# Performance work log

Measured on AMD Instinct MI355X. Metric: run time of the kernel, lower is better.

Reference implementation:

```python
import jax, jax.numpy as jnp
import numpy as np

B, N, E, H = 2, 2048, 768, 12
D = E // H          # head_dim = 64
G = 16              # gate_dim
LN_EPS = 1e-5


def setup_inputs() -> dict:
    key = jax.random.key(0)
    ks = jax.random.split(key, 8)
    s = E ** -0.5
    x = jax.random.normal(ks[0], (B, N, E), jnp.float32)
    # per-head negative decay slopes (ALiBi/TNL-style)
    log_slope = -(2.0 ** (-8.0 * (jnp.arange(H, dtype=jnp.float32) + 1.0) / H))
    Wq = jax.random.normal(ks[1], (E, E), jnp.float32) * s
    Wk = jax.random.normal(ks[2], (E, E), jnp.float32) * s
    Wv = jax.random.normal(ks[3], (E, E), jnp.float32) * s
    Wo = jax.random.normal(ks[4], (E, E), jnp.float32) * s
    Wg1 = jax.random.normal(ks[5], (E, G), jnp.float32) * s
    Wg2 = jax.random.normal(ks[6], (G, E), jnp.float32) * (G ** -0.5)
    ln_w = jnp.ones((E,), jnp.float32)
    ln_b = jnp.zeros((E,), jnp.float32)
    return {"x": x, "log_slope": log_slope, "Wq": Wq, "Wk": Wk, "Wv": Wv,
            "Wo": Wo, "Wg1": Wg1, "Wg2": Wg2, "ln_w": ln_w, "ln_b": ln_b}


def _layernorm(x, w, b):
    mu = jnp.mean(x, axis=-1, keepdims=True)
    var = jnp.mean(jnp.square(x - mu), axis=-1, keepdims=True)
    return (x - mu) * jax.lax.rsqrt(var + LN_EPS) * w + b


def reference(x, log_slope, Wq, Wk, Wv, Wo, Wg1, Wg2, ln_w, ln_b):
    b, n, e = x.shape
    h = log_slope.shape[0]
    d = e // h
    silu = jax.nn.silu
    q = silu(x @ Wq).reshape(b, n, h, d).transpose(0, 2, 1, 3)  # b h n d
    k = silu(x @ Wk).reshape(b, n, h, d).transpose(0, 2, 1, 3)
    v = silu(x @ Wv).reshape(b, n, h, d).transpose(0, 2, 1, 3)

    # exp-decay causal mask: exp(log_slope * (i - j)) for i >= j, else 0
    idx = jnp.arange(n, dtype=jnp.float32)
    diff = idx[:, None] - idx[None, :]                    # n x m
    keep = diff >= 0
    decay = jnp.where(keep,
                      jnp.exp(log_slope[:, None, None] * jnp.maximum(diff, 0.0)),
                      0.0)                                # h n m

    energy = jnp.einsum('bhnd,bhmd->bhnm', q, k) * decay  # b h n m
    out = jnp.einsum('bhnm,bhmd->bhnd', energy, v)        # b h n d
    out = out.transpose(0, 2, 1, 3).reshape(b, n, e)

    gate = jax.nn.sigmoid((x @ Wg1) @ Wg2)                # low-rank output gate
    out = out * gate
    out = out @ Wo
    out = _layernorm(out, ln_w, ln_b)                     # norm_pos='post'
    return out
```

## Files before the change

kernel.cpp:

```cpp
#include <hip/hip_runtime.h>
#include <stdint.h>

#define BB 2
#define NN 2048
#define EE 768
#define HH 12
#define DD 64
#define GG 16

typedef unsigned short u16;
typedef unsigned int u32;
typedef __attribute__((ext_vector_type(8))) short short8;
typedef __attribute__((ext_vector_type(4))) float f32x4;
typedef __attribute__((ext_vector_type(4))) unsigned short u16x4;

__device__ __forceinline__ u16 f2bf(float f) {
  union { float f; u32 u; } a; a.f = f;
  u32 r = a.u + 0x7FFFu + ((a.u >> 16) & 1u);
  return (u16)(r >> 16);
}

__device__ __forceinline__ float silu_f(float v) { return v / (1.f + __expf(-v)); }

__device__ __forceinline__ void gload16(const u16* g, char* l) {
  __builtin_amdgcn_global_load_lds(
      (const __attribute__((address_space(1))) void*)(g),
      (__attribute__((address_space(3))) void*)(l), 16, 0, 0);
}

template<int ROWS>
__device__ __forceinline__ void stage_tile(const u16* __restrict__ gb, int ld, int row0, int col0,
                                           char* lds, int tid) {
  int wid = tid >> 6;
#pragma unroll
  for (int it = 0; it < ROWS / 32; ++it) {
    int c = it * 256 + tid;
    int r = c >> 3;
    int g = (c & 7) ^ (r & 7);
    gload16(gb + (size_t)(row0 + r) * ld + col0 + g * 8,
            lds + (it * 256 + wid * 64) * 16);
  }
}

__device__ __forceinline__ short8 read_frag(const char* lds, int row, int gk) {
  return *(const short8*)(lds + (((row << 3) | (gk ^ (row & 7))) << 4));
}

__global__ __launch_bounds__(256) void xconv_kernel(const float* __restrict__ x, u16* __restrict__ xb) {
  int i = blockIdx.x * 256 + threadIdx.x;
  float4 v = ((const float4*)x)[i];
  u16x4 o;
  o.x = f2bf(v.x); o.y = f2bf(v.y); o.z = f2bf(v.z); o.w = f2bf(v.w);
  ((u16x4*)xb)[i] = o;
}

__global__ __launch_bounds__(256) void wconv_kernel(const float* __restrict__ Wq, const float* __restrict__ Wk,
    const float* __restrict__ Wv, const float* __restrict__ Wo,
    u16* __restrict__ Wqt, u16* __restrict__ Wkt, u16* __restrict__ Wvt, u16* __restrict__ Wot) {
  const float* src; u16* dst;
  int z = blockIdx.z;
  if (z == 0)      { src = Wq; dst = Wqt; }
  else if (z == 1) { src = Wk; dst = Wkt; }
  else if (z == 2) { src = Wv; dst = Wvt; }
  else             { src = Wo; dst = Wot; }
  __shared__ float tb[64][65];
  int k0 = blockIdx.x * 64, n0 = blockIdx.y * 64;
  int tid = threadIdx.x;
#pragma unroll
  for (int i = 0; i < 16; ++i) {
    int idx = i * 256 + tid;
    int r = idx >> 6, c = idx & 63;
    tb[r][c] = src[(size_t)(k0 + r) * EE + n0 + c];
  }
  __syncthreads();
#pragma unroll
  for (int i = 0; i < 16; ++i) {
    int idx = i * 256 + tid;
    int rn = idx >> 6, ck = idx & 63;
    dst[(size_t)(n0 + rn) * EE + k0 + ck] = f2bf(tb[ck][rn]);
  }
}

__global__ __launch_bounds__(256) void tg_kernel(const float* __restrict__ x, const float* __restrict__ Wg1,
                                                 float* __restrict__ tg) {
  int tid = threadIdx.x, lane = tid & 63, wid = tid >> 6;
  int m = blockIdx.x * 4 + wid;
  int col = lane & 15, sl = lane >> 4;
  const float* xr = x + (size_t)m * EE + sl * 192;
  float acc = 0.f;
#pragma unroll 4
  for (int i = 0; i < 48; ++i) {
    float4 xv = ((const float4*)xr)[i];
    int kk = sl * 192 + i * 4;
    acc += xv.x * Wg1[(kk + 0) * GG + col];
    acc += xv.y * Wg1[(kk + 1) * GG + col];
    acc += xv.z * Wg1[(kk + 2) * GG + col];
    acc += xv.w * Wg1[(kk + 3) * GG + col];
  }
  acc += __shfl_down(acc, 32);
  acc += __shfl_down(acc, 16);
  if (lane < 16) tg[(size_t)m * GG + col] = acc;
}

__global__ __launch_bounds__(256) void qkv_gemm(const u16* __restrict__ xb,
    const u16* __restrict__ Wqt, const u16* __restrict__ Wkt, const u16* __restrict__ Wvt,
    u16* __restrict__ qp, u16* __restrict__ kp, u16* __restrict__ vtp) {
  __shared__ __attribute__((aligned(16))) char As[16384];
  __shared__ __attribute__((aligned(16))) char Zs[16384];
  int tid = threadIdx.x, lane = tid & 63, wid = tid >> 6;
  int m0 = blockIdx.x * 128, n0 = blockIdx.y * 128, w = blockIdx.z;
  const u16* Zt = (w == 0) ? Wqt : (w == 1) ? Wkt : Wvt;
  int wm = wid >> 1, wn = wid & 1;
  f32x4 acc[4][4] = {};
  for (int kt = 0; kt < EE / 64; ++kt) {
    __syncthreads();
    stage_tile<128>(xb, EE, m0, kt * 64, As, tid);
    stage_tile<128>(Zt, EE, n0, kt * 64, Zs, tid);
    __syncthreads();
    short8 af[2][4], bfr[2][4];
#pragma unroll
    for (int ds = 0; ds < 2; ++ds) {
      int gk = ds * 4 + (lane >> 4);
#pragma unroll
      for (int i = 0; i < 4; ++i) {
        af[ds][i]  = read_frag(As, wm * 64 + i * 16 + (lane & 15), gk);
        bfr[ds][i] = read_frag(Zs, wn * 64 + i * 16 + (lane & 15), gk);
      }
    }
#pragma unroll
    for (int mi = 0; mi < 4; ++mi)
#pragma unroll
      for (int ni = 0; ni < 4; ++ni) {
        acc[mi][ni] = __builtin_amdgcn_mfma_f32_16x16x32_bf16(af[0][mi], bfr[0][ni], acc[mi][ni], 0, 0, 0);
        acc[mi][ni] = __builtin_amdgcn_mfma_f32_16x16x32_bf16(af[1][mi], bfr[1][ni], acc[mi][ni], 0, 0, 0);
      }
  }
#pragma unroll
  for (int mi = 0; mi < 4; ++mi) {
    int mbase = m0 + wm * 64 + mi * 16 + ((lane >> 4) << 2);
    int bidx = mbase >> 11, nbase = mbase & 2047;
#pragma unroll
    for (int ni = 0; ni < 4; ++ni) {
      int e = n0 + wn * 64 + ni * 16 + (lane & 15);
      int h = e >> 6, d = e & 63;
      if (w < 2) {
        u16* dst = (w == 0 ? qp : kp) + (size_t)(bidx * HH + h) * NN * DD + d;
#pragma unroll
        for (int r = 0; r < 4; ++r)
          dst[(size_t)(nbase + r) * DD] = f2bf(silu_f(acc[mi][ni][r]));
      } else {
        u16x4 pk;
        pk.x = f2bf(silu_f(acc[mi][ni][0]));
        pk.y = f2bf(silu_f(acc[mi][ni][1]));
        pk.z = f2bf(silu_f(acc[mi][ni][2]));
        pk.w = f2bf(silu_f(acc[mi][ni][3]));
        *(u16x4*)(vtp + (size_t)((bidx * HH + h) * DD + d) * NN + nbase) = pk;
      }
    }
  }
}

__global__ __launch_bounds__(256) void attn_kernel(const u16* __restrict__ qp, const u16* __restrict__ kp,
    const u16* __restrict__ vtp, const float* __restrict__ slopes, float* __restrict__ attn) {
  __shared__ __attribute__((aligned(16))) char Ks[8192];
  __shared__ __attribute__((aligned(16))) char Vs[8192];
  __shared__ __attribute__((aligned(16))) char Ps[4][2304];
  int tid = threadIdx.x, lane = tid & 63, wid = tid >> 6;
  int q0 = blockIdx.x * 64;
  int bh = blockIdx.y, b = bh / HH, h = bh % HH;
  float slope = slopes[h];
  const u16* qbh = qp + (size_t)bh * NN * DD;
  const u16* kbh = kp + (size_t)bh * NN * DD;
  const u16* vbh = vtp + (size_t)bh * DD * NN;

  int qrow = q0 + wid * 16 + (lane & 15);
  short8 qf0 = *(const short8*)(qbh + (size_t)qrow * DD + ((lane >> 4) << 3));
  short8 qf1 = *(const short8*)(qbh + (size_t)qrow * DD + 32 + ((lane >> 4) << 3));

  f32x4 oacc[4] = {};
  float window = 30.f / (-slope);
  float jminf = (float)q0 - window;
  int kt_min = (jminf <= 0.f) ? 0 : (((int)jminf) >> 6);
  int kt_max = q0 >> 6;
  char* Pw = Ps[wid];

  for (int kt = kt_min; kt <= kt_max; ++kt) {
    __syncthreads();
    stage_tile<64>(kbh, DD, kt * 64, 0, Ks, tid);
    stage_tile<64>(vbh, NN, 0, kt * 64, Vs, tid);
    __syncthreads();
#pragma unroll
    for (int jt = 0; jt < 4; ++jt) {
      f32x4 s = {};
      s = __builtin_amdgcn_mfma_f32_16x16x32_bf16(qf0, read_frag(Ks, jt * 16 + (lane & 15), (lane >> 4)), s, 0, 0, 0);
      s = __builtin_amdgcn_mfma_f32_16x16x32_bf16(qf1, read_frag(Ks, jt * 16 + (lane & 15), 4 + (lane >> 4)), s, 0, 0, 0);
      int jg = kt * 64 + jt * 16 + (lane & 15);
#pragma unroll
      for (int r = 0; r < 4; ++r) {
        int qi = q0 + wid * 16 + ((lane >> 4) << 2) + r;
        int diff = qi - jg;
        float val = (diff >= 0) ? s[r] * __expf(slope * (float)diff) : 0.f;
        *(u16*)(Pw + ((((lane >> 4) << 2) + r) * 72 + jt * 16 + (lane & 15)) * 2) = f2bf(val);
      }
    }
    __syncthreads();
#pragma unroll
    for (int ks = 0; ks < 2; ++ks) {
      short8 pf = *(const short8*)(Pw + (lane & 15) * 144 + ks * 64 + ((lane >> 4) << 4));
#pragma unroll
      for (int dt = 0; dt < 4; ++dt) {
        oacc[dt] = __builtin_amdgcn_mfma_f32_16x16x32_bf16(
            pf, read_frag(Vs, dt * 16 + (lane & 15), ks * 4 + (lane >> 4)), oacc[dt], 0, 0, 0);
      }
    }
  }
#pragma unroll
  for (int dt = 0; dt < 4; ++dt) {
#pragma unroll
    for (int r = 0; r < 4; ++r) {
      int qi = q0 + wid * 16 + ((lane >> 4) << 2) + r;
      int e = h * 64 + dt * 16 + (lane & 15);
      attn[(size_t)(b * NN + qi) * EE + e] = oacc[dt][r];
    }
  }
}

__global__ __launch_bounds__(256) void gate_kernel(const float* __restrict__ attn, const float* __restrict__ tg,
    const float* __restrict__ Wg2, u16* __restrict__ gated) {
  int m0 = blockIdx.x * 8;
  __shared__ float ts[8][16];
  int tid = threadIdx.x;
  if (tid < 128) ts[tid >> 4][tid & 15] = tg[(size_t)(m0 + (tid >> 4)) * GG + (tid & 15)];
  __syncthreads();
  for (int e = tid; e < EE; e += 256) {
    float wv[16];
#pragma unroll
    for (int g = 0; g < 16; ++g) wv[g] = Wg2[g * EE + e];
#pragma unroll
    for (int r = 0; r < 8; ++r) {
      float gg = 0.f;
#pragma unroll
      for (int g = 0; g < 16; ++g) gg += ts[r][g] * wv[g];
      float sg = 1.f / (1.f + __expf(-gg));
      gated[(size_t)(m0 + r) * EE + e] = f2bf(attn[(size_t)(m0 + r) * EE + e] * sg);
    }
  }
}

__global__ __launch_bounds__(256) void wo_gemm(const u16* __restrict__ A, const u16* __restrict__ Zt,
                                               float* __restrict__ Y) {
  __shared__ __attribute__((aligned(16))) char As[16384];
  __shared__ __attribute__((aligned(16))) char Zs[16384];
  int tid = threadIdx.x, lane = tid & 63, wid = tid >> 6;
  int m0 = blockIdx.x * 128, n0 = blockIdx.y * 128;
  int wm = wid >> 1, wn = wid & 1;
  f32x4 acc[4][4] = {};
  for (int kt = 0; kt < EE / 64; ++kt) {
    __syncthreads();
    stage_tile<128>(A, EE, m0, kt * 64, As, tid);
    stage_tile<128>(Zt, EE, n0, kt * 64, Zs, tid);
    __syncthreads();
    short8 af[2][4], bfr[2][4];
#pragma unroll
    for (int ds = 0; ds < 2; ++ds) {
      int gk = ds * 4 + (lane >> 4);
#pragma unroll
      for (int i = 0; i < 4; ++i) {
        af[ds][i]  = read_frag(As, wm * 64 + i * 16 + (lane & 15), gk);
        bfr[ds][i] = read_frag(Zs, wn * 64 + i * 16 + (lane & 15), gk);
      }
    }
#pragma unroll
    for (int mi = 0; mi < 4; ++mi)
#pragma unroll
      for (int ni = 0; ni < 4; ++ni) {
        acc[mi][ni] = __builtin_amdgcn_mfma_f32_16x16x32_bf16(af[0][mi], bfr[0][ni], acc[mi][ni], 0, 0, 0);
        acc[mi][ni] = __builtin_amdgcn_mfma_f32_16x16x32_bf16(af[1][mi], bfr[1][ni], acc[mi][ni], 0, 0, 0);
      }
  }
#pragma unroll
  for (int mi = 0; mi < 4; ++mi) {
    int mbase = m0 + wm * 64 + mi * 16 + ((lane >> 4) << 2);
#pragma unroll
    for (int ni = 0; ni < 4; ++ni) {
      int e = n0 + wn * 64 + ni * 16 + (lane & 15);
#pragma unroll
      for (int r = 0; r < 4; ++r)
        Y[(size_t)(mbase + r) * EE + e] = acc[mi][ni][r];
    }
  }
}

__global__ __launch_bounds__(256) void ln_kernel(const float* __restrict__ y, const float* __restrict__ w,
    const float* __restrict__ bb, float* __restrict__ out) {
  int m = blockIdx.x, tid = threadIdx.x;
  const float* yr = y + (size_t)m * EE;
  float v0 = yr[tid], v1 = yr[tid + 256], v2 = yr[tid + 512];
  float s = v0 + v1 + v2;
  float s2 = v0 * v0 + v1 * v1 + v2 * v2;
#pragma unroll
  for (int off = 32; off > 0; off >>= 1) {
    s += __shfl_down(s, off);
    s2 += __shfl_down(s2, off);
  }
  __shared__ float ss[4], ssq[4];
  int lane = tid & 63, wid = tid >> 6;
  if (lane == 0) { ss[wid] = s; ssq[wid] = s2; }
  __syncthreads();
  s = ss[0] + ss[1] + ss[2] + ss[3];
  s2 = ssq[0] + ssq[1] + ssq[2] + ssq[3];
  float mu = s * (1.f / 768.f);
  float var = s2 * (1.f / 768.f) - mu * mu;
  float rs = rsqrtf(var + 1e-5f);
  float* orow = out + (size_t)m * EE;
  orow[tid]       = (v0 - mu) * rs * w[tid]       + bb[tid];
  orow[tid + 256] = (v1 - mu) * rs * w[tid + 256] + bb[tid + 256];
  orow[tid + 512] = (v2 - mu) * rs * w[tid + 512] + bb[tid + 512];
}

extern "C" void kernel_launch(void* const* d_in, const int* in_sizes, int n_in,
                              void* d_out, int out_size, void* d_ws, size_t ws_size,
                              hipStream_t stream) {
  (void)in_sizes; (void)n_in; (void)out_size; (void)ws_size;
  const float* x   = (const float*)d_in[0];
  const float* ls  = (const float*)d_in[1];
  const float* Wq  = (const float*)d_in[2];
  const float* Wk  = (const float*)d_in[3];
  const float* Wv  = (const float*)d_in[4];
  const float* Wo  = (const float*)d_in[5];
  const float* Wg1 = (const float*)d_in[6];
  const float* Wg2 = (const float*)d_in[7];
  const float* lnw = (const float*)d_in[8];
  const float* lnb = (const float*)d_in[9];

  char* p = (char*)d_ws;
  u16* xb   = (u16*)(p + 0);
  u16* Wqt  = (u16*)(p + 6291456);
  u16* Wkt  = (u16*)(p + 7471104);
  u16* Wvt  = (u16*)(p + 8650752);
  u16* Wot  = (u16*)(p + 9830400);
  u16* qq   = (u16*)(p + 11010048);
  u16* kk   = (u16*)(p + 17301504);
  u16* vt   = (u16*)(p + 23592960);
  float* tg = (float*)(p + 29884416);
  float* at = (float*)(p + 30146560);
  u16* gated = xb;
  float* yy = (float*)(p + 11010048);
  float* out = (float*)d_out;

  hipLaunchKernelGGL(xconv_kernel, dim3(3072), dim3(256), 0, stream, x, xb);
  hipLaunchKernelGGL(wconv_kernel, dim3(12, 12, 4), dim3(256), 0, stream, Wq, Wk, Wv, Wo, Wqt, Wkt, Wvt, Wot);
  hipLaunchKernelGGL(tg_kernel, dim3(1024), dim3(256), 0, stream, x, Wg1, tg);
  hipLaunchKernelGGL(qkv_gemm, dim3(32, 6, 3), dim3(256), 0, stream, xb, Wqt, Wkt, Wvt, qq, kk, vt);
  hipLaunchKernelGGL(attn_kernel, dim3(32, 24), dim3(256), 0, stream, qq, kk, vt, ls, at);
  hipLaunchKernelGGL(gate_kernel, dim3(512), dim3(256), 0, stream, at, tg, Wg2, gated);
  hipLaunchKernelGGL(wo_gemm, dim3(32, 6), dim3(256), 0, stream, gated, Wot, yy);
  hipLaunchKernelGGL(ln_kernel, dim3(4096), dim3(256), 0, stream, yy, lnw, lnb, out);
}
```

Before: 203.4 us.

## Split attention key range across blocks with atomic accumulation and factored decay

Adds a split-K dimension to the attention grid, where each block handles up to 8 key tiles for one query tile and combines partial outputs with atomicAdd into a pre-zeroed buffer. A new zero kernel clears that buffer first. The per-element exp is factored into a per-row term times a per-column term, and the intra-wave barrier before the P·V step becomes an LDS waitcnt. This targets load imbalance and low parallelism in the causal windowed loop, at the cost of an extra zeroing pass, atomic contention, and float-order nondeterminism; the factored exp may also overflow or underflow for large windows.

```diff
diff --git a/kernel.cpp b/kernel.cpp
--- a/kernel.cpp
+++ b/kernel.cpp
@@ -52,6 +52,10 @@
   u16x4 o;
   o.x = f2bf(v.x); o.y = f2bf(v.y); o.z = f2bf(v.z); o.w = f2bf(v.w);
   ((u16x4*)xb)[i] = o;
+}
+
+__global__ __launch_bounds__(256) void zero_kernel(float4* __restrict__ p) {
+  p[blockIdx.x * 256 + threadIdx.x] = float4{0.f, 0.f, 0.f, 0.f};
 }
 
 __global__ __launch_bounds__(256) void wconv_kernel(const float* __restrict__ Wq, const float* __restrict__ Wk,
@@ -160,50 +164,61 @@
   }
 }
 
+#define CH 8
 __global__ __launch_bounds__(256) void attn_kernel(const u16* __restrict__ qp, const u16* __restrict__ kp,
     const u16* __restrict__ vtp, const float* __restrict__ slopes, float* __restrict__ attn) {
   __shared__ __attribute__((aligned(16))) char Ks[8192];
   __shared__ __attribute__((aligned(16))) char Vs[8192];
   __shared__ __attribute__((aligned(16))) char Ps[4][2304];
   int tid = threadIdx.x, lane = tid & 63, wid = tid >> 6;
-  int q0 = blockIdx.x * 64;
-  int bh = blockIdx.y, b = bh / HH, h = bh % HH;
+  int q0 = blockIdx.y * 64;
+  int bh = blockIdx.z, b = bh / HH, h = bh % HH;
   float slope = slopes[h];
-  const u16* qbh = qp + (size_t)bh * NN * DD;
-  const u16* kbh = kp + (size_t)bh * NN * DD;
-  const u16* vbh = vtp + (size_t)bh * DD * NN;
-
-  int qrow = q0 + wid * 16 + (lane & 15);
-  short8 qf0 = *(const short8*)(qbh + (size_t)qrow * DD + ((lane >> 4) << 3));
-  short8 qf1 = *(const short8*)(qbh + (size_t)qrow * DD + 32 + ((lane >> 4) << 3));
-
-  f32x4 oacc[4] = {};
   float window = 30.f / (-slope);
   float jminf = (float)q0 - window;
   int kt_min = (jminf <= 0.f) ? 0 : (((int)jminf) >> 6);
   int kt_max = q0 >> 6;
+  int k0 = kt_min + (int)blockIdx.x * CH;
+  if (k0 > kt_max) return;
+  int k1 = min(k0 + CH - 1, kt_max);
+  bool single = (kt_max - kt_min) < CH;
+
+  const u16* qbh = qp + (size_t)bh * NN * DD;
+  const u16* kbh = kp + (size_t)bh * NN * DD;
+  const u16* vbh = vtp + (size_t)bh * DD * NN;
+
+  int qbase = q0 + wid * 16 + ((lane >> 4) << 2);
+  int qrow = q0 + wid * 16 + (lane & 15);
+  short8 qf0 = *(const short8*)(qbh + (size_t)qrow * DD + ((lane >> 4) << 3));
+  short8 qf1 = *(const short8*)(qbh + (size_t)qrow * DD + 32 + ((lane >> 4) << 3));
+
+  f32x4 oacc[4] = {};
   char* Pw = Ps[wid];
 
-  for (int kt = kt_min; kt <= kt_max; ++kt) {
+  for (int kt = k0; kt <= k1; ++kt) {
     __syncthreads();
     stage_tile<64>(kbh, DD, kt * 64, 0, Ks, tid);
     stage_tile<64>(vbh, NN, 0, kt * 64, Vs, tid);
     __syncthreads();
+    float t_hi = (float)(kt * 64 + 63);
+    float rex[4];
+#pragma unroll
+    for (int r = 0; r < 4; ++r) rex[r] = __expf(slope * ((float)(qbase + r) - t_hi));
 #pragma unroll
     for (int jt = 0; jt < 4; ++jt) {
       f32x4 s = {};
       s = __builtin_amdgcn_mfma_f32_16x16x32_bf16(qf0, read_frag(Ks, jt * 16 + (lane & 15), (lane >> 4)), s, 0, 0, 0);
       s = __builtin_amdgcn_mfma_f32_16x16x32_bf16(qf1, read_frag(Ks, jt * 16 + (lane & 15), 4 + (lane >> 4)), s, 0, 0, 0);
       int jg = kt * 64 + jt * 16 + (lane & 15);
+      float cex = __expf(slope * (t_hi - (float)jg));
 #pragma unroll
       for (int r = 0; r < 4; ++r) {
-        int qi = q0 + wid * 16 + ((lane >> 4) << 2) + r;
-        int diff = qi - jg;
-        float val = (diff >= 0) ? s[r] * __expf(slope * (float)diff) : 0.f;
+        int diff = qbase + r - jg;
+        float val = (diff >= 0) ? s[r] * rex[r] * cex : 0.f;
         *(u16*)(Pw + ((((lane >> 4) << 2) + r) * 72 + jt * 16 + (lane & 15)) * 2) = f2bf(val);
       }
     }
-    __syncthreads();
+    __asm__ volatile("s_waitcnt lgkmcnt(0)" ::: "memory");
 #pragma unroll
     for (int ks = 0; ks < 2; ++ks) {
       short8 pf = *(const short8*)(Pw + (lane & 15) * 144 + ks * 64 + ((lane >> 4) << 4));
@@ -218,9 +233,11 @@
   for (int dt = 0; dt < 4; ++dt) {
 #pragma unroll
     for (int r = 0; r < 4; ++r) {
-      int qi = q0 + wid * 16 + ((lane >> 4) << 2) + r;
+      int qi = qbase + r;
       int e = h * 64 + dt * 16 + (lane & 15);
-      attn[(size_t)(b * NN + qi) * EE + e] = oacc[dt][r];
+      float* dst = attn + (size_t)(b * NN + qi) * EE + e;
+      if (single) *dst = oacc[dt][r];
+      else atomicAdd(dst, oacc[dt][r]);
     }
   }
 }
@@ -349,10 +366,11 @@
   float* out = (float*)d_out;
 
   hipLaunchKernelGGL(xconv_kernel, dim3(3072), dim3(256), 0, stream, x, xb);
+  hipLaunchKernelGGL(zero_kernel, dim3(3072), dim3(256), 0, stream, (float4*)at);
   hipLaunchKernelGGL(wconv_kernel, dim3(12, 12, 4), dim3(256), 0, stream, Wq, Wk, Wv, Wo, Wqt, Wkt, Wvt, Wot);
   hipLaunchKernelGGL(tg_kernel, dim3(1024), dim3(256), 0, stream, x, Wg1, tg);
   hipLaunchKernelGGL(qkv_gemm, dim3(32, 6, 3), dim3(256), 0, stream, xb, Wqt, Wkt, Wvt, qq, kk, vt);
-  hipLaunchKernelGGL(attn_kernel, dim3(32, 24), dim3(256), 0, stream, qq, kk, vt, ls, at);
+  hipLaunchKernelGGL(attn_kernel, dim3(4, 32, 24), dim3(256), 0, stream, qq, kk, vt, ls, at);
   hipLaunchKernelGGL(gate_kernel, dim3(512), dim3(256), 0, stream, at, tg, Wg2, gated);
   hipLaunchKernelGGL(wo_gemm, dim3(32, 6), dim3(256), 0, stream, gated, Wot, yy);
   hipLaunchKernelGGL(ln_kernel, dim3(4096), dim3(256), 0, stream, yy, lnw, lnb, out);
```

New measurement: 206.4 us. No clear change (+1.5%).
